# Kernel tuning notes

Hardware: AMD Instinct MI355X
Metric: run time of the kernel (lower is better)

Reference implementation:

```python
import jax, jax.numpy as jnp
from jax import lax
import numpy as np

N_BASIS = 256
N_FREQ = 128
N_TIME = 8
LAM = 0.2
LR = 1e-3
B1, B2, EPS = 0.9, 0.999, 1e-8
CONV_TOL = 1e-3


def setup_inputs() -> dict:
    key = jax.random.key(0)
    k1, k2 = jax.random.split(key)
    spec = jax.random.normal(k1, (32, N_FREQ, 256), dtype=jnp.float32)
    basis = jax.random.normal(k2, (N_FREQ * N_TIME, N_BASIS), dtype=jnp.float32)
    return {"spec": spec, "basis": basis, "n_iter_coef": 30, "pad": 0, "stride": 4}


def normalize01(x):
    # torch normalize01 with dims=-1, keepdims
    xmin = x.min(axis=-1, keepdims=True)
    xmax = x.max(axis=-1, keepdims=True)
    return (x - xmin) / (xmax - xmin)


def _response(x, basis, n_iter):
    # x: [B, D]; Adam-optimize coef [B, N_BASIS] for n_iter steps with the
    # same early-stop rule as the torch code (frozen via a done flag).
    B = x.shape[0]
    sig = jnp.std(x, ddof=1)  # torch .std() is unbiased over all elements

    def loss_fn(coef):
        pred = coef @ basis.T                      # [B, D]
        mse = jnp.mean((pred - x) ** 2)
        return mse + LAM * sig * jnp.mean(jnp.abs(coef / sig))

    coef0 = jnp.full((B, N_BASIS), 0.5 / N_BASIS, dtype=jnp.float32)
    m0 = jnp.zeros_like(coef0)
    v0 = jnp.zeros_like(coef0)

    def body(carry, _):
        coef, m, v, t, old_loss, done = carry
        loss, g = jax.value_and_grad(loss_fn)(coef)
        t_new = t + 1.0
        m_new = B1 * m + (1.0 - B1) * g
        v_new = B2 * v + (1.0 - B2) * g * g
        mhat = m_new / (1.0 - B1 ** t_new)
        vhat = v_new / (1.0 - B2 ** t_new)
        coef_new = coef - LR * mhat / (jnp.sqrt(vhat) + EPS)
        conv = jnp.abs(old_loss - loss) / old_loss < CONV_TOL
        sel = lambda a, b: jnp.where(done, a, b)
        new_carry = (
            sel(coef, coef_new),
            sel(m, m_new),
            sel(v, v_new),
            jnp.where(done, t, t_new),
            jnp.where(done, old_loss, loss),
            done | conv,
        )
        return new_carry, None

    init = (coef0, m0, v0, jnp.float32(0.0), jnp.float32(1e-10), jnp.array(False))
    (coef, _, _, _, _, _), _ = lax.scan(body, init, None, length=n_iter)
    return coef  # detached in torch


def reference(spec, basis, n_iter_coef, pad, stride):
    if spec.ndim == 2:
        spec = spec[None, ...]
    B, F, T = spec.shape
    spec_ = jnp.pad(spec, ((0, 0), (0, 0), (pad, pad)))
    starts = np.arange(0, T - N_TIME + 1, stride)          # window start frames
    idx = starts[:, None] + np.arange(N_TIME)              # [W, N_TIME]
    wins = spec_[:, :, idx]                                # [B, F, W, N_TIME]
    x = jnp.transpose(wins, (2, 0, 1, 3)).reshape(len(starts), B, F * N_TIME)
    x = normalize01(x)                                     # per row of [B, D]
    coef = jax.vmap(lambda xw: _response(xw, basis, n_iter_coef))(x)  # [W, B, N_BASIS]
    return jnp.transpose(coef, (1, 2, 0))                  # [B, N_BASIS, W]
```

## Files before the change

### kernel.cpp

```cpp
#include <hip/hip_runtime.h>
#include <math.h>

#define NB     256
#define NF     128
#define FT     1024
#define NW     63
#define TORIG  256
#define MAXIT  48
#define RPB    8
#define NBLK   4
#define GRID   256

using f32x4  = __attribute__((ext_vector_type(4))) float;
using bf16x8 = __attribute__((ext_vector_type(8))) short;

__device__ __forceinline__ int xidx(int k2, int cg, int row) {
    return (k2 * 512 + row * 64 + (cg ^ row)) * 4;
}

__device__ __forceinline__ unsigned bf16_hi(float x) {
    const unsigned u = __float_as_uint(x);
    return (u + 0x7fffu + ((u >> 16) & 1u)) >> 16;
}

__global__ __launch_bounds__(512, 2) void window_kernel(
    const float* __restrict__ spec,
    const float* __restrict__ basis,
    float* __restrict__ G,
    const int* __restrict__ p_niter,
    const int* __restrict__ p_pad,
    const int* __restrict__ p_stride,
    double* __restrict__ sxbuf,
    double* __restrict__ gpart,
    unsigned int* __restrict__ gcnt,
    float* __restrict__ out)
{
    __shared__ __align__(16) float s_p0[RPB * 2048];
    __shared__ __align__(16) float s_xn[RPB * FT];
    __shared__ __align__(16) short A0[16 * NB];
    __shared__ __align__(16) short A1[16 * NB];
    __shared__ float  s_gred[2][NB];
    __shared__ float  s_mn[RPB], s_rng[RPB];
    __shared__ double s_dred[8];
    __shared__ float  s_redq[2][8], s_redr[2][8];
    __shared__ unsigned int s_wcnt[2];
    __shared__ int    s_stop[2];

    const int bid = blockIdx.x;
    const int yy  = bid >> 3;
    const int q   = yy & 3;
    const int w   = (bid & 7) + 8 * (yy >> 2);
    const int tid = threadIdx.x;
    const int ks  = tid >> 6;
    const int kg  = tid & 63;
    const int r   = kg >> 3;
    const int cgo = 8 * ks + (kg & 7);
    const int n_iter = p_niter[0];
    const int t0     = w * p_stride[0] - p_pad[0];
    unsigned int* gbar = gcnt + MAXIT * NW;

    {
        const int c = tid & 255, jh = tid >> 8;
        float acc = 0.f;
        const float* bp = basis + (size_t)(jh * 512) * NB;
        #pragma unroll 16
        for (int j = 0; j < 512; ++j)
            acc = fmaf(bp[j * NB + bid], bp[j * NB + c], acc);
        s_gred[jh][c] = acc;
        __syncthreads();
        if (jh == 0) G[(size_t)bid * NB + c] = s_gred[0][c] + s_gred[1][c];
    }
    __threadfence();
    __syncthreads();
    if (tid == 0) atomicAdd(gbar, 1u);
    if (w >= NW) return;

    #pragma unroll
    for (int i = 0; i < 16; ++i) {
        const int e = i * 512 + tid;
        const int b = e >> 10, jj = e & 1023;
        const int f = jj >> 3, t = jj & 7, tq = t0 + t;
        s_xn[b * FT + jj] = (tq >= 0 && tq < TORIG)
            ? spec[((size_t)(q * RPB + b) * NF + f) * TORIG + tq] : 0.f;
    }
    __syncthreads();
    {
        float mn = __builtin_inff(), mx = -__builtin_inff();
        #pragma unroll
        for (int i = 0; i < 16; ++i) {
            const float v = s_xn[ks * FT + i * 64 + kg];
            mn = fminf(mn, v); mx = fmaxf(mx, v);
        }
        #pragma unroll
        for (int off = 32; off; off >>= 1) {
            mn = fminf(mn, __shfl_down(mn, off));
            mx = fmaxf(mx, __shfl_down(mx, off));
        }
        if (kg == 0) { s_mn[ks] = mn; s_rng[ks] = mx - mn; }
    }
    __syncthreads();
    double sx2p = 0.0;
    #pragma unroll
    for (int i = 0; i < 16; ++i) {
        const int e = i * 512 + tid;
        const int b = e >> 10, jj = e & 1023;
        const float v = (s_xn[b * FT + jj] - s_mn[b]) / s_rng[b];
        s_xn[b * FT + jj] = v;
        sx2p += (double)v * (double)v;
    }
    #pragma unroll
    for (int off = 32; off; off >>= 1) sx2p += __shfl_down(sx2p, off);
    if (kg == 0) s_dred[ks] = sx2p;
    __syncthreads();
    if (tid == 0) {
        double s = 0.0;
        #pragma unroll
        for (int i = 0; i < 8; ++i) s += s_dred[i];
        sxbuf[w * NBLK + q] = s;
        __threadfence();
    }

    float xbp[RPB][4];
    #pragma unroll
    for (int b = 0; b < RPB; ++b)
        #pragma unroll
        for (int j = 0; j < 4; ++j) xbp[b][j] = 0.f;
    for (int i0 = 0; i0 < 128; i0 += 4) {
        const int jj = ks * 128 + i0;
        float4 bv[4];
        #pragma unroll
        for (int t = 0; t < 4; ++t)
            bv[t] = *(const float4*)(basis + (size_t)(jj + t) * NB + 4 * kg);
        #pragma unroll
        for (int b = 0; b < RPB; ++b) {
            const float4 x4 = *(const float4*)&s_xn[b * FT + jj];
            xbp[b][0] = fmaf(x4.x, bv[0].x, fmaf(x4.y, bv[1].x, fmaf(x4.z, bv[2].x, fmaf(x4.w, bv[3].x, xbp[b][0]))));
            xbp[b][1] = fmaf(x4.x, bv[0].y, fmaf(x4.y, bv[1].y, fmaf(x4.z, bv[2].y, fmaf(x4.w, bv[3].y, xbp[b][1]))));
            xbp[b][2] = fmaf(x4.x, bv[0].z, fmaf(x4.y, bv[1].z, fmaf(x4.z, bv[2].z, fmaf(x4.w, bv[3].z, xbp[b][2]))));
            xbp[b][3] = fmaf(x4.x, bv[0].w, fmaf(x4.y, bv[1].w, fmaf(x4.z, bv[2].w, fmaf(x4.w, bv[3].w, xbp[b][3]))));
        }
    }
    __syncthreads();
    #pragma unroll
    for (int b = 0; b < RPB; ++b)
        *(float4*)&s_p0[xidx(ks, kg, b)] =
            make_float4(xbp[b][0], xbp[b][1], xbp[b][2], xbp[b][3]);
    __syncthreads();
    float xBo[4] = {0.f, 0.f, 0.f, 0.f};
    #pragma unroll
    for (int k2 = 0; k2 < 8; ++k2) {
        const float4 p4 = *(const float4*)&s_p0[xidx(k2, cgo, r)];
        xBo[0] += p4.x; xBo[1] += p4.y; xBo[2] += p4.z; xBo[3] += p4.w;
    }
    *(float4*)&s_xn[r * NB + 4 * cgo] = make_float4(xBo[0], xBo[1], xBo[2], xBo[3]);

    if (tid == 0) {
        while (__hip_atomic_load(gbar, __ATOMIC_ACQUIRE, __HIP_MEMORY_SCOPE_AGENT) < (unsigned)GRID)
            __builtin_amdgcn_s_sleep(1);
    }
    if (tid == 64) { s_wcnt[0] = 0; s_wcnt[1] = 0; s_stop[0] = 0; s_stop[1] = 0; }
    __syncthreads();

    const int lr  = kg & 15;
    const int lh  = kg >> 4;
    const int hlf = kg >> 5;

    float xB[8];
    #pragma unroll
    for (int T = 0; T < 2; ++T)
        #pragma unroll
        for (int t = 0; t < 4; ++t)
            xB[4*T + t] = s_xn[(4*(lh & 1) + t) * NB + 32*ks + 16*T + lr];

    bf16x8 Gh[8][2], Gl[8][2];
    {
        const float* gp = G + (size_t)(8 * lh) * NB + 32 * ks + lr;
        #pragma unroll
        for (int kk = 0; kk < 8; ++kk)
            #pragma unroll
            for (int T = 0; T < 2; ++T)
                #pragma unroll
                for (int b = 0; b < 8; ++b) {
                    const float gv = gp[(size_t)(32*kk + b) * NB + 16*T];
                    const unsigned hb = bf16_hi(gv);
                    const float    hf = __uint_as_float(hb << 16);
                    const unsigned lb = bf16_hi(gv - hf);
                    Gh[kk][T][b] = (short)hb;
                    Gl[kk][T][b] = (short)lb;
                }
    }

    unsigned awaddr[8];
    #pragma unroll
    for (int T = 0; T < 2; ++T)
        #pragma unroll
        for (int t = 0; t < 4; ++t) {
            const int hr  = 4*(lh & 1) + t;
            const int col = 32*ks + 16*T + lr;
            awaddr[4*T + t] = (unsigned)((((hr * NB + col) ^ ((hr & 7) << 3)) * 2)
                                         + (hlf ? 4096 : 0));
        }
    const unsigned abase = (unsigned)(((lr * NB + lh * 8) ^ ((lr & 7) << 3)) * 2);

    const float C0 = 0.5f / 256.f;
    float cf[8], cfp[8], m_[8], v_[8];
    #pragma unroll
    for (int j = 0; j < 8; ++j) { cf[j] = C0; cfp[j] = C0; m_[j] = 0.f; v_[j] = 0.f; }
    {
        const short vh  = (short)bf16_hi(C0);
        const short val = hlf ? (short)0 : vh;
        #pragma unroll
        for (int j = 0; j < 8; ++j)
            *(short*)((char*)A0 + awaddr[j]) = val;
    }
    float b1p = 1.f, b2p = 1.f;
    float old_loss = 1e-10f;
    double sxtot = 0.0;
    const float c1c = 2.f / 32768.f, c2c = 0.2f / 8192.f;
    int use_prev = 0;

    for (int it = 0; it < n_iter; ++it) {
        const int p = it & 1;
        const char* rdb = (const char*)(p ? A1 : A0);
        char*       wrb = (char*)(p ? A0 : A1);

        __syncthreads();

        f32x4 a1[2], a2[2];
        const f32x4 z4 = {0.f, 0.f, 0.f, 0.f};
        a1[0] = z4; a1[1] = z4; a2[0] = z4; a2[1] = z4;
        #pragma unroll
        for (int kk = 0; kk < 8; ++kk) {
            const bf16x8 af = *(const bf16x8*)(rdb + (abase ^ (unsigned)(kk << 6)));
            a1[0] = __builtin_amdgcn_mfma_f32_16x16x32_bf16(af, Gh[kk][0], a1[0], 0, 0, 0);
            a2[0] = __builtin_amdgcn_mfma_f32_16x16x32_bf16(af, Gl[kk][0], a2[0], 0, 0, 0);
            a1[1] = __builtin_amdgcn_mfma_f32_16x16x32_bf16(af, Gh[kk][1], a1[1], 0, 0, 0);
            a2[1] = __builtin_amdgcn_mfma_f32_16x16x32_bf16(af, Gl[kk][1], a2[1], 0, 0, 0);
        }
        float a4[8];
        #pragma unroll
        for (int T = 0; T < 2; ++T)
            #pragma unroll
            for (int t = 0; t < 4; ++t) {
                const float s = a1[T][t] + a2[T][t];
                a4[4*T + t] = s + __shfl_xor(s, 32);
            }

        if (tid == 64 && it >= 2) {
            const int itc = it - 2;
            while (__hip_atomic_load(&gcnt[itc * NW + w], __ATOMIC_ACQUIRE,
                                     __HIP_MEMORY_SCOPE_AGENT) < (unsigned)NBLK)
                __builtin_amdgcn_s_sleep(1);
            const size_t pbm = ((size_t)itc * NW + w) * NBLK;
            double Qt = 0.0, Rt = 0.0;
            #pragma unroll
            for (int i = 0; i < NBLK; ++i) {
                Qt += gpart[(pbm + i) * 2 + 0];
                Rt += gpart[(pbm + i) * 2 + 1];
            }
            if (itc == 0)
                sxtot = sxbuf[w * NBLK + 0] + sxbuf[w * NBLK + 1] +
                        sxbuf[w * NBLK + 2] + sxbuf[w * NBLK + 3];
            const float loss = (float)((Qt + sxtot) / 32768.0 + 0.2 * (Rt / 8192.0));
            const float stat = fabsf(old_loss - loss) / old_loss;
            old_loss = loss;
            s_stop[p] = (stat < 1e-3f) ? 1 : 0;
        }

        __syncthreads();

        if (s_stop[p]) { use_prev = 1; break; }

        if (it + 1 < n_iter) {
            float qc = 0.f, rr = 0.f;
            #pragma unroll
            for (int j = 0; j < 8; ++j) {
                qc += cf[j] * (a4[j] - 2.f * xB[j]);
                rr += fabsf(cf[j]);
            }
            if (kg >= 32) { qc = 0.f; rr = 0.f; }
            #pragma unroll
            for (int off = 32; off; off >>= 1) {
                qc += __shfl_down(qc, off);
                rr += __shfl_down(rr, off);
            }
            if (kg == 0) {
                s_redq[p][ks] = qc; s_redr[p][ks] = rr;
                __threadfence_block();
                const unsigned old = __hip_atomic_fetch_add(&s_wcnt[p], 1u,
                                        __ATOMIC_ACQ_REL, __HIP_MEMORY_SCOPE_WORKGROUP);
                if (old == 7u) {
                    float Q = 0.f, R = 0.f;
                    #pragma unroll
                    for (int i = 0; i < 8; ++i) { Q += s_redq[p][i]; R += s_redr[p][i]; }
                    s_wcnt[p] = 0u;
                    const size_t pb = ((size_t)it * NW + w) * NBLK;
                    gpart[(pb + q) * 2 + 0] = (double)Q;
                    gpart[(pb + q) * 2 + 1] = (double)R;
                    __hip_atomic_fetch_add(&gcnt[it * NW + w], 1u,
                                           __ATOMIC_RELEASE, __HIP_MEMORY_SCOPE_AGENT);
                }
            }
        }

        b1p *= 0.9f; b2p *= 0.999f;
        const float rb1 = __builtin_amdgcn_rcpf(1.f - b1p);
        const float rb2 = __builtin_amdgcn_rcpf(1.f - b2p);
        #pragma unroll
        for (int j = 0; j < 8; ++j) {
            const float c_ = cf[j];
            cfp[j] = c_;
            const float sgn = (c_ > 0.f) ? 1.f : ((c_ < 0.f) ? -1.f : 0.f);
            const float gg = c1c * (a4[j] - xB[j]) + c2c * sgn;
            m_[j] = 0.9f * m_[j] + 0.1f * gg;
            v_[j] = 0.999f * v_[j] + 0.001f * gg * gg;
            const float den = __builtin_amdgcn_sqrtf(v_[j] * rb2) + 1e-8f;
            cf[j] = c_ - 1e-3f * (m_[j] * rb1) * __builtin_amdgcn_rcpf(den);
        }

        #pragma unroll
        for (int j = 0; j < 8; ++j) {
            const unsigned hb = bf16_hi(cf[j]);
            const float    hf = __uint_as_float(hb << 16);
            const unsigned lb = bf16_hi(cf[j] - hf);
            *(short*)(wrb + awaddr[j]) = (short)(hlf ? lb : hb);
        }
    }

    if (!use_prev && n_iter >= 2) {
        if (tid == 64) {
            const int itc = n_iter - 2;
            while (__hip_atomic_load(&gcnt[itc * NW + w], __ATOMIC_ACQUIRE,
                                     __HIP_MEMORY_SCOPE_AGENT) < (unsigned)NBLK)
                __builtin_amdgcn_s_sleep(1);
            const size_t pbm = ((size_t)itc * NW + w) * NBLK;
            double Qt = 0.0, Rt = 0.0;
            #pragma unroll
            for (int i = 0; i < NBLK; ++i) {
                Qt += gpart[(pbm + i) * 2 + 0];
                Rt += gpart[(pbm + i) * 2 + 1];
            }
            if (itc == 0)
                sxtot = sxbuf[w * NBLK + 0] + sxbuf[w * NBLK + 1] +
                        sxbuf[w * NBLK + 2] + sxbuf[w * NBLK + 3];
            const float loss = (float)((Qt + sxtot) / 32768.0 + 0.2 * (Rt / 8192.0));
            const float stat = fabsf(old_loss - loss) / old_loss;
            s_stop[0] = (stat < 1e-3f) ? 1 : 0;
        }
        __syncthreads();
        use_prev = s_stop[0];
    }

    if (kg < 32) {
        #pragma unroll
        for (int T = 0; T < 2; ++T)
            #pragma unroll
            for (int t = 0; t < 4; ++t)
                out[((size_t)(q * RPB + 4*lh + t) * NB + 32*ks + 16*T + lr) * NW + w] =
                    use_prev ? cfp[4*T + t] : cf[4*T + t];
    }
}

extern "C" void kernel_launch(void* const* d_in, const int* in_sizes, int n_in,
                              void* d_out, int out_size, void* d_ws, size_t ws_size,
                              hipStream_t stream)
{
    const float* spec   = (const float*)d_in[0];
    const float* basis  = (const float*)d_in[1];
    const int* p_niter  = (const int*)d_in[2];
    const int* p_pad    = (const int*)d_in[3];
    const int* p_stride = (const int*)d_in[4];
    float* out = (float*)d_out;

    char* ws = (char*)d_ws;
    float*        G     = (float*)ws;
    double*       sxbuf = (double*)(ws + 262144);
    double*       gpart = (double*)(ws + 266240);
    unsigned int* gcnt  = (unsigned int*)(ws + 266240 + 193536);

    hipMemsetAsync(gcnt, 0, (MAXIT * NW + 1) * sizeof(unsigned int), stream);
    window_kernel<<<dim3(GRID), dim3(512), 0, stream>>>(
        spec, basis, G, p_niter, p_pad, p_stride, sxbuf, gpart, gcnt, out);
}
```

Baseline: 291.2 us.

## Process all 32 rows of a window in one block, dropping cross-block loss sync

```diff
diff --git a/kernel.cpp b/kernel.cpp
--- a/kernel.cpp
+++ b/kernel.cpp
@@ -6,9 +6,7 @@
 #define FT     1024
 #define NW     63
 #define TORIG  256
-#define MAXIT  48
 #define RPB    8
-#define NBLK   4
 #define GRID   256
 
 using f32x4  = __attribute__((ext_vector_type(4))) float;
@@ -23,41 +21,36 @@
     return (u + 0x7fffu + ((u >> 16) & 1u)) >> 16;
 }
 
-__global__ __launch_bounds__(512, 2) void window_kernel(
+__global__ __launch_bounds__(512, 1) void window_kernel(
     const float* __restrict__ spec,
     const float* __restrict__ basis,
     float* __restrict__ G,
     const int* __restrict__ p_niter,
     const int* __restrict__ p_pad,
     const int* __restrict__ p_stride,
-    double* __restrict__ sxbuf,
-    double* __restrict__ gpart,
-    unsigned int* __restrict__ gcnt,
+    unsigned int* __restrict__ gbar,
     float* __restrict__ out)
 {
-    __shared__ __align__(16) float s_p0[RPB * 2048];
-    __shared__ __align__(16) float s_xn[RPB * FT];
-    __shared__ __align__(16) short A0[16 * NB];
-    __shared__ __align__(16) short A1[16 * NB];
+    __shared__ __align__(16) char arena[98304];
+    short* const A0   = (short*)arena;
+    short* const A1   = (short*)(arena + 32768);
+    float* const s_xn = (float*)(arena + 65536);
+    float* const s_p0 = (float*)arena;
+    __shared__ __align__(16) float s_xb[32 * NB];
     __shared__ float  s_gred[2][NB];
     __shared__ float  s_mn[RPB], s_rng[RPB];
     __shared__ double s_dred[8];
+    __shared__ double s_sx;
     __shared__ float  s_redq[2][8], s_redr[2][8];
-    __shared__ unsigned int s_wcnt[2];
     __shared__ int    s_stop[2];
 
     const int bid = blockIdx.x;
-    const int yy  = bid >> 3;
-    const int q   = yy & 3;
-    const int w   = (bid & 7) + 8 * (yy >> 2);
     const int tid = threadIdx.x;
     const int ks  = tid >> 6;
     const int kg  = tid & 63;
     const int r   = kg >> 3;
     const int cgo = 8 * ks + (kg & 7);
     const int n_iter = p_niter[0];
-    const int t0     = w * p_stride[0] - p_pad[0];
-    unsigned int* gbar = gcnt + MAXIT * NW;
 
     {
         const int c = tid & 255, jh = tid >> 8;
@@ -73,104 +66,103 @@
     __threadfence();
     __syncthreads();
     if (tid == 0) atomicAdd(gbar, 1u);
-    if (w >= NW) return;
-
-    #pragma unroll
-    for (int i = 0; i < 16; ++i) {
-        const int e = i * 512 + tid;
-        const int b = e >> 10, jj = e & 1023;
-        const int f = jj >> 3, t = jj & 7, tq = t0 + t;
-        s_xn[b * FT + jj] = (tq >= 0 && tq < TORIG)
-            ? spec[((size_t)(q * RPB + b) * NF + f) * TORIG + tq] : 0.f;
-    }
-    __syncthreads();
-    {
-        float mn = __builtin_inff(), mx = -__builtin_inff();
+    if (bid >= NW) return;
+
+    const int w  = bid;
+    const int t0 = w * p_stride[0] - p_pad[0];
+    if (tid == 0) s_sx = 0.0;
+
+    #pragma unroll 1
+    for (int rg = 0; rg < 4; ++rg) {
         #pragma unroll
         for (int i = 0; i < 16; ++i) {
-            const float v = s_xn[ks * FT + i * 64 + kg];
-            mn = fminf(mn, v); mx = fmaxf(mx, v);
-        }
-        #pragma unroll
-        for (int off = 32; off; off >>= 1) {
-            mn = fminf(mn, __shfl_down(mn, off));
-            mx = fmaxf(mx, __shfl_down(mx, off));
-        }
-        if (kg == 0) { s_mn[ks] = mn; s_rng[ks] = mx - mn; }
-    }
-    __syncthreads();
-    double sx2p = 0.0;
-    #pragma unroll
-    for (int i = 0; i < 16; ++i) {
-        const int e = i * 512 + tid;
-        const int b = e >> 10, jj = e & 1023;
-        const float v = (s_xn[b * FT + jj] - s_mn[b]) / s_rng[b];
-        s_xn[b * FT + jj] = v;
-        sx2p += (double)v * (double)v;
-    }
-    #pragma unroll
-    for (int off = 32; off; off >>= 1) sx2p += __shfl_down(sx2p, off);
-    if (kg == 0) s_dred[ks] = sx2p;
-    __syncthreads();
-    if (tid == 0) {
-        double s = 0.0;
-        #pragma unroll
-        for (int i = 0; i < 8; ++i) s += s_dred[i];
-        sxbuf[w * NBLK + q] = s;
-        __threadfence();
-    }
-
-    float xbp[RPB][4];
-    #pragma unroll
-    for (int b = 0; b < RPB; ++b)
-        #pragma unroll
-        for (int j = 0; j < 4; ++j) xbp[b][j] = 0.f;
-    for (int i0 = 0; i0 < 128; i0 += 4) {
-        const int jj = ks * 128 + i0;
-        float4 bv[4];
-        #pragma unroll
-        for (int t = 0; t < 4; ++t)
-            bv[t] = *(const float4*)(basis + (size_t)(jj + t) * NB + 4 * kg);
-        #pragma unroll
-        for (int b = 0; b < RPB; ++b) {
-            const float4 x4 = *(const float4*)&s_xn[b * FT + jj];
-            xbp[b][0] = fmaf(x4.x, bv[0].x, fmaf(x4.y, bv[1].x, fmaf(x4.z, bv[2].x, fmaf(x4.w, bv[3].x, xbp[b][0]))));
-            xbp[b][1] = fmaf(x4.x, bv[0].y, fmaf(x4.y, bv[1].y, fmaf(x4.z, bv[2].y, fmaf(x4.w, bv[3].y, xbp[b][1]))));
-            xbp[b][2] = fmaf(x4.x, bv[0].z, fmaf(x4.y, bv[1].z, fmaf(x4.z, bv[2].z, fmaf(x4.w, bv[3].z, xbp[b][2]))));
-            xbp[b][3] = fmaf(x4.x, bv[0].w, fmaf(x4.y, bv[1].w, fmaf(x4.z, bv[2].w, fmaf(x4.w, bv[3].w, xbp[b][3]))));
-        }
-    }
-    __syncthreads();
-    #pragma unroll
-    for (int b = 0; b < RPB; ++b)
-        *(float4*)&s_p0[xidx(ks, kg, b)] =
-            make_float4(xbp[b][0], xbp[b][1], xbp[b][2], xbp[b][3]);
-    __syncthreads();
-    float xBo[4] = {0.f, 0.f, 0.f, 0.f};
-    #pragma unroll
-    for (int k2 = 0; k2 < 8; ++k2) {
-        const float4 p4 = *(const float4*)&s_p0[xidx(k2, cgo, r)];
-        xBo[0] += p4.x; xBo[1] += p4.y; xBo[2] += p4.z; xBo[3] += p4.w;
-    }
-    *(float4*)&s_xn[r * NB + 4 * cgo] = make_float4(xBo[0], xBo[1], xBo[2], xBo[3]);
+            const int e = i * 512 + tid;
+            const int b = e >> 10, jj = e & 1023;
+            const int f = jj >> 3, t = jj & 7, tq = t0 + t;
+            s_xn[b * FT + jj] = (tq >= 0 && tq < TORIG)
+                ? spec[((size_t)(rg * RPB + b) * NF + f) * TORIG + tq] : 0.f;
+        }
+        __syncthreads();
+        {
+            float mn = __builtin_inff(), mx = -__builtin_inff();
+            #pragma unroll
+            for (int i = 0; i < 16; ++i) {
+                const float v = s_xn[ks * FT + i * 64 + kg];
+                mn = fminf(mn, v); mx = fmaxf(mx, v);
+            }
+            #pragma unroll
+            for (int off = 32; off; off >>= 1) {
+                mn = fminf(mn, __shfl_down(mn, off));
+                mx = fmaxf(mx, __shfl_down(mx, off));
+            }
+            if (kg == 0) { s_mn[ks] = mn; s_rng[ks] = mx - mn; }
+        }
+        __syncthreads();
+        double sx2p = 0.0;
+        #pragma unroll
+        for (int i = 0; i < 16; ++i) {
+            const int e = i * 512 + tid;
+            const int b = e >> 10, jj = e & 1023;
+            const float v = (s_xn[b * FT + jj] - s_mn[b]) / s_rng[b];
+            s_xn[b * FT + jj] = v;
+            sx2p += (double)v * (double)v;
+        }
+        #pragma unroll
+        for (int off = 32; off; off >>= 1) sx2p += __shfl_down(sx2p, off);
+        if (kg == 0) s_dred[ks] = sx2p;
+        __syncthreads();
+        if (tid == 0) {
+            double s = 0.0;
+            #pragma unroll
+            for (int i = 0; i < 8; ++i) s += s_dred[i];
+            s_sx += s;
+        }
+
+        float xbp[RPB][4];
+        #pragma unroll
+        for (int b = 0; b < RPB; ++b)
+            #pragma unroll
+            for (int j = 0; j < 4; ++j) xbp[b][j] = 0.f;
+        for (int i0 = 0; i0 < 128; i0 += 4) {
+            const int jj = ks * 128 + i0;
+            float4 bv[4];
+            #pragma unroll
+            for (int t = 0; t < 4; ++t)
+                bv[t] = *(const float4*)(basis + (size_t)(jj + t) * NB + 4 * kg);
+            #pragma unroll
+            for (int b = 0; b < RPB; ++b) {
+                const float4 x4 = *(const float4*)&s_xn[b * FT + jj];
+                xbp[b][0] = fmaf(x4.x, bv[0].x, fmaf(x4.y, bv[1].x, fmaf(x4.z, bv[2].x, fmaf(x4.w, bv[3].x, xbp[b][0]))));
+                xbp[b][1] = fmaf(x4.x, bv[0].y, fmaf(x4.y, bv[1].y, fmaf(x4.z, bv[2].y, fmaf(x4.w, bv[3].y, xbp[b][1]))));
+                xbp[b][2] = fmaf(x4.x, bv[0].z, fmaf(x4.y, bv[1].z, fmaf(x4.z, bv[2].z, fmaf(x4.w, bv[3].z, xbp[b][2]))));
+                xbp[b][3] = fmaf(x4.x, bv[0].w, fmaf(x4.y, bv[1].w, fmaf(x4.z, bv[2].w, fmaf(x4.w, bv[3].w, xbp[b][3]))));
+            }
+        }
+        __syncthreads();
+        #pragma unroll
+        for (int b = 0; b < RPB; ++b)
+            *(float4*)&s_p0[xidx(ks, kg, b)] =
+                make_float4(xbp[b][0], xbp[b][1], xbp[b][2], xbp[b][3]);
+        __syncthreads();
+        float xBo[4] = {0.f, 0.f, 0.f, 0.f};
+        #pragma unroll
+        for (int k2 = 0; k2 < 8; ++k2) {
+            const float4 p4 = *(const float4*)&s_p0[xidx(k2, cgo, r)];
+            xBo[0] += p4.x; xBo[1] += p4.y; xBo[2] += p4.z; xBo[3] += p4.w;
+        }
+        *(float4*)&s_xb[(size_t)(rg * RPB + r) * NB + 4 * cgo] =
+            make_float4(xBo[0], xBo[1], xBo[2], xBo[3]);
+    }
 
     if (tid == 0) {
         while (__hip_atomic_load(gbar, __ATOMIC_ACQUIRE, __HIP_MEMORY_SCOPE_AGENT) < (unsigned)GRID)
             __builtin_amdgcn_s_sleep(1);
     }
-    if (tid == 64) { s_wcnt[0] = 0; s_wcnt[1] = 0; s_stop[0] = 0; s_stop[1] = 0; }
+    if (tid == 64) { s_stop[0] = 0; s_stop[1] = 0; }
     __syncthreads();
 
-    const int lr  = kg & 15;
-    const int lh  = kg >> 4;
-    const int hlf = kg >> 5;
-
-    float xB[8];
-    #pragma unroll
-    for (int T = 0; T < 2; ++T)
-        #pragma unroll
-        for (int t = 0; t < 4; ++t)
-            xB[4*T + t] = s_xn[(4*(lh & 1) + t) * NB + 32*ks + 16*T + lr];
+    const int lr = kg & 15;
+    const int lh = kg >> 4;
 
     bf16x8 Gh[8][2], Gl[8][2];
     {
@@ -181,7 +173,7 @@
             for (int T = 0; T < 2; ++T)
                 #pragma unroll
                 for (int b = 0; b < 8; ++b) {
-                    const float gv = gp[(size_t)(32*kk + b) * NB + 16*T];
+                    const float gv = gp[(size_t)(32 * kk + b) * NB + 16 * T];
                     const unsigned hb = bf16_hi(gv);
                     const float    hf = __uint_as_float(hb << 16);
                     const unsigned lb = bf16_hi(gv - hf);
@@ -190,28 +182,37 @@
                 }
     }
 
-    unsigned awaddr[8];
+    float xB[16];
     #pragma unroll
-    for (int T = 0; T < 2; ++T)
-        #pragma unroll
-        for (int t = 0; t < 4; ++t) {
-            const int hr  = 4*(lh & 1) + t;
-            const int col = 32*ks + 16*T + lr;
-            awaddr[4*T + t] = (unsigned)((((hr * NB + col) ^ ((hr & 7) << 3)) * 2)
-                                         + (hlf ? 4096 : 0));
-        }
-    const unsigned abase = (unsigned)(((lr * NB + lh * 8) ^ ((lr & 7) << 3)) * 2);
+    for (int pp = 0; pp < 2; ++pp)
+        #pragma unroll
+        for (int T = 0; T < 2; ++T)
+            #pragma unroll
+            for (int t = 0; t < 4; ++t)
+                xB[pp * 8 + T * 4 + t] =
+                    s_xb[(size_t)(16 * pp + 4 * lh + t) * NB + 32 * ks + 16 * T + lr];
+
+    const int base0 = lr * 256 + 8 * lh;
+    const int swz   = (lr & 7) << 3;
 
     const float C0 = 0.5f / 256.f;
-    float cf[8], cfp[8], m_[8], v_[8];
+    float cf[16], m_[16], v_[16];
     #pragma unroll
-    for (int j = 0; j < 8; ++j) { cf[j] = C0; cfp[j] = C0; m_[j] = 0.f; v_[j] = 0.f; }
+    for (int j = 0; j < 16; ++j) { cf[j] = C0; m_[j] = 0.f; v_[j] = 0.f; }
     {
-        const short vh  = (short)bf16_hi(C0);
-        const short val = hlf ? (short)0 : vh;
-        #pragma unroll
-        for (int j = 0; j < 8; ++j)
-            *(short*)((char*)A0 + awaddr[j]) = val;
+        const short vh = (short)bf16_hi(C0);
+        #pragma unroll
+        for (int pp = 0; pp < 2; ++pp)
+            #pragma unroll
+            for (int T = 0; T < 2; ++T)
+                #pragma unroll
+                for (int t = 0; t < 4; ++t) {
+                    const int rr = 16 * pp + 4 * lh + t;
+                    const int cc = 32 * ks + 16 * T + lr;
+                    const int wb = ((rr * 256 + cc) ^ ((rr & 7) << 3)) << 1;
+                    *(short*)((char*)A0 + wb)         = vh;
+                    *(short*)((char*)A0 + wb + 16384) = 0;
+                }
     }
     float b1p = 1.f, b2p = 1.f;
     float old_loss = 1e-10f;
@@ -226,41 +227,36 @@
 
         __syncthreads();
 
-        f32x4 a1[2], a2[2];
+        f32x4 acc[2][2];
         const f32x4 z4 = {0.f, 0.f, 0.f, 0.f};
-        a1[0] = z4; a1[1] = z4; a2[0] = z4; a2[1] = z4;
+        acc[0][0] = z4; acc[0][1] = z4; acc[1][0] = z4; acc[1][1] = z4;
         #pragma unroll
         for (int kk = 0; kk < 8; ++kk) {
-            const bf16x8 af = *(const bf16x8*)(rdb + (abase ^ (unsigned)(kk << 6)));
-            a1[0] = __builtin_amdgcn_mfma_f32_16x16x32_bf16(af, Gh[kk][0], a1[0], 0, 0, 0);
-            a2[0] = __builtin_amdgcn_mfma_f32_16x16x32_bf16(af, Gl[kk][0], a2[0], 0, 0, 0);
-            a1[1] = __builtin_amdgcn_mfma_f32_16x16x32_bf16(af, Gh[kk][1], a1[1], 0, 0, 0);
-            a2[1] = __builtin_amdgcn_mfma_f32_16x16x32_bf16(af, Gl[kk][1], a2[1], 0, 0, 0);
-        }
-        float a4[8];
-        #pragma unroll
-        for (int T = 0; T < 2; ++T)
-            #pragma unroll
-            for (int t = 0; t < 4; ++t) {
-                const float s = a1[T][t] + a2[T][t];
-                a4[4*T + t] = s + __shfl_xor(s, 32);
-            }
+            #pragma unroll
+            for (int pp = 0; pp < 2; ++pp) {
+                const int o = base0 + pp * 4096 + kk * 32;
+                const bf16x8 ah = *(const bf16x8*)(rdb + ((o ^ swz) << 1));
+                const bf16x8 al = *(const bf16x8*)(rdb + (((o + 8192) ^ swz) << 1));
+                acc[pp][0] = __builtin_amdgcn_mfma_f32_16x16x32_bf16(ah, Gh[kk][0], acc[pp][0], 0, 0, 0);
+                acc[pp][1] = __builtin_amdgcn_mfma_f32_16x16x32_bf16(ah, Gh[kk][1], acc[pp][1], 0, 0, 0);
+                acc[pp][0] = __builtin_amdgcn_mfma_f32_16x16x32_bf16(al, Gh[kk][0], acc[pp][0], 0, 0, 0);
+                acc[pp][1] = __builtin_amdgcn_mfma_f32_16x16x32_bf16(al, Gh[kk][1], acc[pp][1], 0, 0, 0);
+                acc[pp][0] = __builtin_amdgcn_mfma_f32_16x16x32_bf16(ah, Gl[kk][0], acc[pp][0], 0, 0, 0);
+                acc[pp][1] = __builtin_amdgcn_mfma_f32_16x16x32_bf16(ah, Gl[kk][1], acc[pp][1], 0, 0, 0);
+                acc[pp][0] = __builtin_amdgcn_mfma_f32_16x16x32_bf16(al, Gl[kk][0], acc[pp][0], 0, 0, 0);
+                acc[pp][1] = __builtin_amdgcn_mfma_f32_16x16x32_bf16(al, Gl[kk][1], acc[pp][1], 0, 0, 0);
+            }
+        }
 
         if (tid == 64 && it >= 2) {
             const int itc = it - 2;
-            while (__hip_atomic_load(&gcnt[itc * NW + w], __ATOMIC_ACQUIRE,
-                                     __HIP_MEMORY_SCOPE_AGENT) < (unsigned)NBLK)
-                __builtin_amdgcn_s_sleep(1);
-            const size_t pbm = ((size_t)itc * NW + w) * NBLK;
             double Qt = 0.0, Rt = 0.0;
             #pragma unroll
-            for (int i = 0; i < NBLK; ++i) {
-                Qt += gpart[(pbm + i) * 2 + 0];
-                Rt += gpart[(pbm + i) * 2 + 1];
-            }
-            if (itc == 0)
-                sxtot = sxbuf[w * NBLK + 0] + sxbuf[w * NBLK + 1] +
-                        sxbuf[w * NBLK + 2] + sxbuf[w * NBLK + 3];
+            for (int i = 0; i < 8; ++i) {
+                Qt += (double)s_redq[p][i];
+                Rt += (double)s_redr[p][i];
+            }
+            if (itc == 0) sxtot = s_sx;
             const float loss = (float)((Qt + sxtot) / 32768.0 + 0.2 * (Rt / 8192.0));
             const float stat = fabsf(old_loss - loss) / old_loss;
             old_loss = loss;
@@ -272,46 +268,30 @@
         if (s_stop[p]) { use_prev = 1; break; }
 
         if (it + 1 < n_iter) {
-            float qc = 0.f, rr = 0.f;
-            #pragma unroll
-            for (int j = 0; j < 8; ++j) {
-                qc += cf[j] * (a4[j] - 2.f * xB[j]);
-                rr += fabsf(cf[j]);
-            }
-            if (kg >= 32) { qc = 0.f; rr = 0.f; }
+            float qc = 0.f, rr_ = 0.f;
+            #pragma unroll
+            for (int j = 0; j < 16; ++j) {
+                const float a4v = acc[j >> 3][(j >> 2) & 1][j & 3];
+                qc += cf[j] * (a4v - 2.f * xB[j]);
+                rr_ += fabsf(cf[j]);
+            }
             #pragma unroll
             for (int off = 32; off; off >>= 1) {
-                qc += __shfl_down(qc, off);
-                rr += __shfl_down(rr, off);
-            }
-            if (kg == 0) {
-                s_redq[p][ks] = qc; s_redr[p][ks] = rr;
-                __threadfence_block();
-                const unsigned old = __hip_atomic_fetch_add(&s_wcnt[p], 1u,
-                                        __ATOMIC_ACQ_REL, __HIP_MEMORY_SCOPE_WORKGROUP);
-                if (old == 7u) {
-                    float Q = 0.f, R = 0.f;
-                    #pragma unroll
-                    for (int i = 0; i < 8; ++i) { Q += s_redq[p][i]; R += s_redr[p][i]; }
-                    s_wcnt[p] = 0u;
-                    const size_t pb = ((size_t)it * NW + w) * NBLK;
-                    gpart[(pb + q) * 2 + 0] = (double)Q;
-                    gpart[(pb + q) * 2 + 1] = (double)R;
-                    __hip_atomic_fetch_add(&gcnt[it * NW + w], 1u,
-                                           __ATOMIC_RELEASE, __HIP_MEMORY_SCOPE_AGENT);
-                }
-            }
+                qc  += __shfl_down(qc, off);
+                rr_ += __shfl_down(rr_, off);
+            }
+            if (kg == 0) { s_redq[p][ks] = qc; s_redr[p][ks] = rr_; }
         }
 
         b1p *= 0.9f; b2p *= 0.999f;
         const float rb1 = __builtin_amdgcn_rcpf(1.f - b1p);
         const float rb2 = __builtin_amdgcn_rcpf(1.f - b2p);
         #pragma unroll
-        for (int j = 0; j < 8; ++j) {
-            const float c_ = cf[j];
-            cfp[j] = c_;
+        for (int j = 0; j < 16; ++j) {
+            const float a4v = acc[j >> 3][(j >> 2) & 1][j & 3];
+            const float c_  = cf[j];
             const float sgn = (c_ > 0.f) ? 1.f : ((c_ < 0.f) ? -1.f : 0.f);
-            const float gg = c1c * (a4[j] - xB[j]) + c2c * sgn;
+            const float gg  = c1c * (a4v - xB[j]) + c2c * sgn;
             m_[j] = 0.9f * m_[j] + 0.1f * gg;
             v_[j] = 0.999f * v_[j] + 0.001f * gg * gg;
             const float den = __builtin_amdgcn_sqrtf(v_[j] * rb2) + 1e-8f;
@@ -319,30 +299,34 @@
         }
 
         #pragma unroll
-        for (int j = 0; j < 8; ++j) {
-            const unsigned hb = bf16_hi(cf[j]);
-            const float    hf = __uint_as_float(hb << 16);
-            const unsigned lb = bf16_hi(cf[j] - hf);
-            *(short*)(wrb + awaddr[j]) = (short)(hlf ? lb : hb);
-        }
+        for (int pp = 0; pp < 2; ++pp)
+            #pragma unroll
+            for (int T = 0; T < 2; ++T)
+                #pragma unroll
+                for (int t = 0; t < 4; ++t) {
+                    const int j  = pp * 8 + T * 4 + t;
+                    const int rr = 16 * pp + 4 * lh + t;
+                    const int cc = 32 * ks + 16 * T + lr;
+                    const int wb = ((rr * 256 + cc) ^ ((rr & 7) << 3)) << 1;
+                    const unsigned hb = bf16_hi(cf[j]);
+                    const float    hf = __uint_as_float(hb << 16);
+                    const unsigned lb = bf16_hi(cf[j] - hf);
+                    *(short*)(wrb + wb)         = (short)hb;
+                    *(short*)(wrb + wb + 16384) = (short)lb;
+                }
     }
 
     if (!use_prev && n_iter >= 2) {
         if (tid == 64) {
             const int itc = n_iter - 2;
-            while (__hip_atomic_load(&gcnt[itc * NW + w], __ATOMIC_ACQUIRE,
-                                     __HIP_MEMORY_SCOPE_AGENT) < (unsigned)NBLK)
-                __builtin_amdgcn_s_sleep(1);
-            const size_t pbm = ((size_t)itc * NW + w) * NBLK;
+            const int pc  = itc & 1;
             double Qt = 0.0, Rt = 0.0;
             #pragma unroll
-            for (int i = 0; i < NBLK; ++i) {
-                Qt += gpart[(pbm + i) * 2 + 0];
-                Rt += gpart[(pbm + i) * 2 + 1];
-            }
-            if (itc == 0)
-                sxtot = sxbuf[w * NBLK + 0] + sxbuf[w * NBLK + 1] +
-                        sxbuf[w * NBLK + 2] + sxbuf[w * NBLK + 3];
+            for (int i = 0; i < 8; ++i) {
+                Qt += (double)s_redq[pc][i];
+                Rt += (double)s_redr[pc][i];
+            }
+            if (itc == 0) sxtot = s_sx;
             const float loss = (float)((Qt + sxtot) / 32768.0 + 0.2 * (Rt / 8192.0));
             const float stat = fabsf(old_loss - loss) / old_loss;
             s_stop[0] = (stat < 1e-3f) ? 1 : 0;
@@ -351,13 +335,23 @@
         use_prev = s_stop[0];
     }
 
-    if (kg < 32) {
-        #pragma unroll
-        for (int T = 0; T < 2; ++T)
-            #pragma unroll
-            for (int t = 0; t < 4; ++t)
-                out[((size_t)(q * RPB + 4*lh + t) * NB + 32*ks + 16*T + lr) * NW + w] =
-                    use_prev ? cfp[4*T + t] : cf[4*T + t];
+    {
+        const float rb1e = __builtin_amdgcn_rcpf(1.f - b1p);
+        const float rb2e = __builtin_amdgcn_rcpf(1.f - b2p);
+        #pragma unroll
+        for (int pp = 0; pp < 2; ++pp)
+            #pragma unroll
+            for (int T = 0; T < 2; ++T)
+                #pragma unroll
+                for (int t = 0; t < 4; ++t) {
+                    const int j = pp * 8 + T * 4 + t;
+                    float val = cf[j];
+                    if (use_prev) {
+                        const float den = __builtin_amdgcn_sqrtf(v_[j] * rb2e) + 1e-8f;
+                        val += 1e-3f * (m_[j] * rb1e) * __builtin_amdgcn_rcpf(den);
+                    }
+                    out[((size_t)(16 * pp + 4 * lh + t) * NB + 32 * ks + 16 * T + lr) * NW + w] = val;
+                }
     }
 }
 
@@ -373,12 +367,10 @@
     float* out = (float*)d_out;
 
     char* ws = (char*)d_ws;
-    float*        G     = (float*)ws;
-    double*       sxbuf = (double*)(ws + 262144);
-    double*       gpart = (double*)(ws + 266240);
-    unsigned int* gcnt  = (unsigned int*)(ws + 266240 + 193536);
-
-    hipMemsetAsync(gcnt, 0, (MAXIT * NW + 1) * sizeof(unsigned int), stream);
+    float*        G    = (float*)ws;
+    unsigned int* gbar = (unsigned int*)(ws + 262144);
+
+    hipMemsetAsync(gbar, 0, sizeof(unsigned int), stream);
     window_kernel<<<dim3(GRID), dim3(512), 0, stream>>>(
-        spec, basis, G, p_niter, p_pad, p_stride, sxbuf, gpart, gcnt, out);
+        spec, basis, G, p_niter, p_pad, p_stride, gbar, out);
 }
```

Result: slower. 419.3 us (+44.0%).

## Stream pre-split bf16 Gram matrix from global instead of holding it in registers

Applied to the files above, without the earlier changes.

```diff
diff --git a/kernel.cpp b/kernel.cpp
--- a/kernel.cpp
+++ b/kernel.cpp
@@ -10,12 +10,17 @@
 #define RPB    8
 #define NBLK   4
 #define GRID   256
+#define GCNT_N (8 * MAXIT * 8)
 
 using f32x4  = __attribute__((ext_vector_type(4))) float;
 using bf16x8 = __attribute__((ext_vector_type(8))) short;
 
 __device__ __forceinline__ int xidx(int k2, int cg, int row) {
     return (k2 * 512 + row * 64 + (cg ^ row)) * 4;
+}
+
+__device__ __forceinline__ int gidx(int it, int w) {
+    return (w & 7) * (MAXIT * 8) + it * 8 + (w >> 3);
 }
 
 __device__ __forceinline__ unsigned bf16_hi(float x) {
@@ -26,7 +31,8 @@
 __global__ __launch_bounds__(512, 2) void window_kernel(
     const float* __restrict__ spec,
     const float* __restrict__ basis,
-    float* __restrict__ G,
+    short* __restrict__ Ghi,
+    short* __restrict__ Glo,
     const int* __restrict__ p_niter,
     const int* __restrict__ p_pad,
     const int* __restrict__ p_stride,
@@ -56,8 +62,7 @@
     const int r   = kg >> 3;
     const int cgo = 8 * ks + (kg & 7);
     const int n_iter = p_niter[0];
-    const int t0     = w * p_stride[0] - p_pad[0];
-    unsigned int* gbar = gcnt + MAXIT * NW;
+    unsigned int* gbar = gcnt + GCNT_N;
 
     {
         const int c = tid & 255, jh = tid >> 8;
@@ -68,12 +73,20 @@
             acc = fmaf(bp[j * NB + bid], bp[j * NB + c], acc);
         s_gred[jh][c] = acc;
         __syncthreads();
-        if (jh == 0) G[(size_t)bid * NB + c] = s_gred[0][c] + s_gred[1][c];
+        if (jh == 0) {
+            const float g = s_gred[0][c] + s_gred[1][c];
+            const unsigned hb = bf16_hi(g);
+            const float    hf = __uint_as_float(hb << 16);
+            Ghi[(size_t)bid * NB + c] = (short)hb;
+            Glo[(size_t)bid * NB + c] = (short)bf16_hi(g - hf);
+        }
     }
     __threadfence();
     __syncthreads();
     if (tid == 0) atomicAdd(gbar, 1u);
     if (w >= NW) return;
+
+    const int t0 = w * p_stride[0] - p_pad[0];
 
     #pragma unroll
     for (int i = 0; i < 16; ++i) {
@@ -172,23 +185,9 @@
         for (int t = 0; t < 4; ++t)
             xB[4*T + t] = s_xn[(4*(lh & 1) + t) * NB + 32*ks + 16*T + lr];
 
-    bf16x8 Gh[8][2], Gl[8][2];
-    {
-        const float* gp = G + (size_t)(8 * lh) * NB + 32 * ks + lr;
-        #pragma unroll
-        for (int kk = 0; kk < 8; ++kk)
-            #pragma unroll
-            for (int T = 0; T < 2; ++T)
-                #pragma unroll
-                for (int b = 0; b < 8; ++b) {
-                    const float gv = gp[(size_t)(32*kk + b) * NB + 16*T];
-                    const unsigned hb = bf16_hi(gv);
-                    const float    hf = __uint_as_float(hb << 16);
-                    const unsigned lb = bf16_hi(gv - hf);
-                    Gh[kk][T][b] = (short)hb;
-                    Gl[kk][T][b] = (short)lb;
-                }
-    }
+    const int c0 = 32 * ks + lr;
+    const short* ghp = Ghi + (size_t)c0 * NB + 8 * lh;
+    const short* glp = Glo + (size_t)c0 * NB + 8 * lh;
 
     unsigned awaddr[8];
     #pragma unroll
@@ -229,13 +228,17 @@
         f32x4 a1[2], a2[2];
         const f32x4 z4 = {0.f, 0.f, 0.f, 0.f};
         a1[0] = z4; a1[1] = z4; a2[0] = z4; a2[1] = z4;
-        #pragma unroll
+        #pragma unroll 2
         for (int kk = 0; kk < 8; ++kk) {
-            const bf16x8 af = *(const bf16x8*)(rdb + (abase ^ (unsigned)(kk << 6)));
-            a1[0] = __builtin_amdgcn_mfma_f32_16x16x32_bf16(af, Gh[kk][0], a1[0], 0, 0, 0);
-            a2[0] = __builtin_amdgcn_mfma_f32_16x16x32_bf16(af, Gl[kk][0], a2[0], 0, 0, 0);
-            a1[1] = __builtin_amdgcn_mfma_f32_16x16x32_bf16(af, Gh[kk][1], a1[1], 0, 0, 0);
-            a2[1] = __builtin_amdgcn_mfma_f32_16x16x32_bf16(af, Gl[kk][1], a2[1], 0, 0, 0);
+            const bf16x8 Gh0 = *(const bf16x8*)(ghp + 32 * kk);
+            const bf16x8 Gl0 = *(const bf16x8*)(glp + 32 * kk);
+            const bf16x8 Gh1 = *(const bf16x8*)(ghp + 4096 + 32 * kk);
+            const bf16x8 Gl1 = *(const bf16x8*)(glp + 4096 + 32 * kk);
+            const bf16x8 af  = *(const bf16x8*)(rdb + (abase ^ (unsigned)(kk << 6)));
+            a1[0] = __builtin_amdgcn_mfma_f32_16x16x32_bf16(af, Gh0, a1[0], 0, 0, 0);
+            a2[0] = __builtin_amdgcn_mfma_f32_16x16x32_bf16(af, Gl0, a2[0], 0, 0, 0);
+            a1[1] = __builtin_amdgcn_mfma_f32_16x16x32_bf16(af, Gh1, a1[1], 0, 0, 0);
+            a2[1] = __builtin_amdgcn_mfma_f32_16x16x32_bf16(af, Gl1, a2[1], 0, 0, 0);
         }
         float a4[8];
         #pragma unroll
@@ -248,7 +251,7 @@
 
         if (tid == 64 && it >= 2) {
             const int itc = it - 2;
-            while (__hip_atomic_load(&gcnt[itc * NW + w], __ATOMIC_ACQUIRE,
+            while (__hip_atomic_load(&gcnt[gidx(itc, w)], __ATOMIC_ACQUIRE,
                                      __HIP_MEMORY_SCOPE_AGENT) < (unsigned)NBLK)
                 __builtin_amdgcn_s_sleep(1);
             const size_t pbm = ((size_t)itc * NW + w) * NBLK;
@@ -297,7 +300,7 @@
                     const size_t pb = ((size_t)it * NW + w) * NBLK;
                     gpart[(pb + q) * 2 + 0] = (double)Q;
                     gpart[(pb + q) * 2 + 1] = (double)R;
-                    __hip_atomic_fetch_add(&gcnt[it * NW + w], 1u,
+                    __hip_atomic_fetch_add(&gcnt[gidx(it, w)], 1u,
                                            __ATOMIC_RELEASE, __HIP_MEMORY_SCOPE_AGENT);
                 }
             }
@@ -330,7 +333,7 @@
     if (!use_prev && n_iter >= 2) {
         if (tid == 64) {
             const int itc = n_iter - 2;
-            while (__hip_atomic_load(&gcnt[itc * NW + w], __ATOMIC_ACQUIRE,
+            while (__hip_atomic_load(&gcnt[gidx(itc, w)], __ATOMIC_ACQUIRE,
                                      __HIP_MEMORY_SCOPE_AGENT) < (unsigned)NBLK)
                 __builtin_amdgcn_s_sleep(1);
             const size_t pbm = ((size_t)itc * NW + w) * NBLK;
@@ -373,12 +376,13 @@
     float* out = (float*)d_out;
 
     char* ws = (char*)d_ws;
-    float*        G     = (float*)ws;
+    short*        Ghi   = (short*)ws;
+    short*        Glo   = (short*)(ws + 131072);
     double*       sxbuf = (double*)(ws + 262144);
     double*       gpart = (double*)(ws + 266240);
     unsigned int* gcnt  = (unsigned int*)(ws + 266240 + 193536);
 
-    hipMemsetAsync(gcnt, 0, (MAXIT * NW + 1) * sizeof(unsigned int), stream);
+    hipMemsetAsync(gcnt, 0, (GCNT_N + 1) * sizeof(unsigned int), stream);
     window_kernel<<<dim3(GRID), dim3(512), 0, stream>>>(
-        spec, basis, G, p_niter, p_pad, p_stride, sxbuf, gpart, gcnt, out);
-}
+        spec, basis, Ghi, Glo, p_niter, p_pad, p_stride, sxbuf, gpart, gcnt, out);
+}
```

Result: slower. 474.9 us (+63.1%).
